# Performance work log

Measured on AMD Instinct MI355X. Metric: run time of the kernel, lower is better.

The kernel has to match this reference:

```python
import jax, jax.numpy as jnp
import numpy as np

EMBED_DIM = 1024
ZDIM = 128
STD = 0.02


def setup_inputs() -> dict:
    key = jax.random.key(0)
    ks = jax.random.split(key, 12)
    T, S, B, E, Z = 2048, 2048, 4, EMBED_DIM, ZDIM
    return {
        "query": jax.random.normal(ks[0], (T, B, E), jnp.float32),
        "key": jax.random.normal(ks[1], (S, B, E), jnp.float32),
        "Wq": jax.random.normal(ks[2], (2 * E + Z, E), jnp.float32) * STD,
        "bq": jnp.zeros((2 * E + Z,), jnp.float32),
        "Wk": jax.random.normal(ks[3], (Z, E), jnp.float32) * STD,
        "bk": jnp.zeros((Z,), jnp.float32),
        "Wv": jax.random.normal(ks[4], (E, E), jnp.float32) * STD,
        "bv": jnp.zeros((E,), jnp.float32),
        "Wh": jax.random.normal(ks[5], (E, E), jnp.float32) * STD,
        "bh": jnp.zeros((E,), jnp.float32),
        "gamma": jax.random.normal(ks[6], (2, Z), jnp.float32) * STD,
        "beta": jnp.zeros((2, Z), jnp.float32),
    }


def reference(query, key, Wq, bq, Wk, bk, Wv, bv, Wh, bh, gamma, beta):
    E, Z = EMBED_DIM, ZDIM
    scaling = Z ** (-0.5)
    # base: [T, B, 2E+Z]
    base = jnp.einsum('tbe,fe->tbf', query, Wq) + bq
    u = jax.nn.sigmoid(base[..., :E])                      # [T,B,E] output gate
    rq = jax.nn.silu(base[..., E:])                        # [T,B,E+Z]
    r = rq[..., :E]                                        # [T,B,E]
    q = rq[..., E:] * gamma[0] + beta[0]                   # [T,B,Z]
    k = jax.nn.silu(jnp.einsum('sbe,ze->sbz', key, Wk) + bk) * gamma[1] + beta[1]  # [S,B,Z]
    v = jax.nn.silu(jnp.einsum('sbe,fe->sbf', key, Wv) + bv)                       # [S,B,E]
    # softmax attention over context dim
    qk = jnp.einsum('tbz,sbz->bts', q * scaling, k)        # [B,T,S]
    attn = jax.nn.softmax(qk, axis=-1)
    h = jnp.einsum('bts,sbf->tbf', attn, v)                # [T,B,E]
    h = jnp.tanh(jnp.einsum('tbe,fe->tbf', h * r, Wh) + bh)
    out = query + u * (h - query)                          # addcmul
    return out
```

## Files before the change

kernel.cpp:

```cpp
#include <hip/hip_runtime.h>
#include <cstdint>
#include <cstddef>

using short8  = __attribute__((ext_vector_type(8))) short;
using floatx4 = __attribute__((ext_vector_type(4))) float;

#define DEV __device__ __forceinline__

DEV float u2f(unsigned short u){
  union { unsigned int i; float f; } c; c.i = ((unsigned int)u) << 16; return c.f;
}
DEV unsigned short f2u(float f){
  union { float f; unsigned int i; } c; c.f = f;
  unsigned int i = c.i;
  i += 0x7fffu + ((i >> 16) & 1u);
  return (unsigned short)(i >> 16);
}
DEV float sigmoidf_(float x){ return 1.0f / (1.0f + __expf(-x)); }
DEV float siluf_(float x){ return x / (1.0f + __expf(-x)); }

#define ASYNC_LD16(g, l) __builtin_amdgcn_global_load_lds( \
    (const __attribute__((address_space(1))) unsigned int*)(g), \
    (__attribute__((address_space(3))) unsigned int*)(l), 16, 0, 0)

constexpr float SCALING = 0.088388347648318447f;

__global__ __launch_bounds__(256) void cast_f32_bf16(
    const float* __restrict__ in, unsigned short* __restrict__ out, int n)
{
  const int i = (blockIdx.x * 256 + threadIdx.x) * 4;
  if (i >= n) return;
  const float4 v = *(const float4*)(in + i);
  ushort4 o;
  o.x = f2u(v.x); o.y = f2u(v.y); o.z = f2u(v.z); o.w = f2u(v.w);
  *(ushort4*)(out + i) = o;
}

__global__ __launch_bounds__(256) void softmax_rows(float* __restrict__ logits)
{
  const long long rb = blockIdx.x;
  float* row = logits + rb * 2048;
  unsigned short* prow = (unsigned short*)logits + rb * 4096;
  const int tid = threadIdx.x;
  const int lane = tid & 63, wv = tid >> 6;

  const float4 a = *(const float4*)(row + tid * 4);
  const float4 b = *(const float4*)(row + 1024 + tid * 4);

  float mx = fmaxf(fmaxf(fmaxf(a.x,a.y),fmaxf(a.z,a.w)),
                   fmaxf(fmaxf(b.x,b.y),fmaxf(b.z,b.w)));
  #pragma unroll
  for (int m = 32; m >= 1; m >>= 1) mx = fmaxf(mx, __shfl_xor(mx, m));
  __shared__ float red[4];
  if (lane == 0) red[wv] = mx;
  __syncthreads();
  mx = fmaxf(fmaxf(red[0], red[1]), fmaxf(red[2], red[3]));

  float e[8];
  e[0]=__expf(a.x-mx); e[1]=__expf(a.y-mx); e[2]=__expf(a.z-mx); e[3]=__expf(a.w-mx);
  e[4]=__expf(b.x-mx); e[5]=__expf(b.y-mx); e[6]=__expf(b.z-mx); e[7]=__expf(b.w-mx);
  float sm = 0.f;
  #pragma unroll
  for (int i = 0; i < 8; i++) sm += e[i];
  #pragma unroll
  for (int m = 32; m >= 1; m >>= 1) sm += __shfl_xor(sm, m);
  __syncthreads();
  if (lane == 0) red[wv] = sm;
  __syncthreads();
  const float inv = 1.0f / (red[0] + red[1] + red[2] + red[3]);

  ushort4 o0, o1;
  o0.x=f2u(e[0]*inv); o0.y=f2u(e[1]*inv); o0.z=f2u(e[2]*inv); o0.w=f2u(e[3]*inv);
  o1.x=f2u(e[4]*inv); o1.y=f2u(e[5]*inv); o1.z=f2u(e[6]*inv); o1.w=f2u(e[7]*inv);
  *(ushort4*)(prow + tid * 4) = o0;
  *(ushort4*)(prow + 1024 + tid * 4) = o1;
}

template<int EPI>
__global__ __launch_bounds__(256, 2)
void gemm_bt(const unsigned short* __restrict__ A, long long bsA, int lda,
             const unsigned short* __restrict__ Bm, long long bsB, int ldb,
             int K,
             const float* __restrict__ bias,
             const float* __restrict__ gam,
             const float* __restrict__ bet,
             float* __restrict__ f0,
             unsigned short* __restrict__ b0,
             unsigned short* __restrict__ b1,
             const unsigned short* __restrict__ rmul,
             const float* __restrict__ qin,
             const float* __restrict__ uin)
{
  __shared__ __align__(16) unsigned short As[128][64];
  __shared__ __align__(16) unsigned short Bs[128][64];

  const int tid = threadIdx.x;
  const int bm = blockIdx.x, bn = blockIdx.y, bz = blockIdx.z;
  const unsigned short* Ag = A  + (long long)bz * bsA;
  const unsigned short* Bg = Bm + (long long)bz * bsB;
  const int row0 = bm * 128;
  const int col0 = bn * 128;

  const int lane = tid & 63;
  const int wv   = tid >> 6;
  const int wm   = (wv & 1) * 64;
  const int wn   = (wv >> 1) * 64;
  const int lr   = lane & 15;
  const int lq   = lane >> 4;
  const int r7   = lr & 7;

  const unsigned short* gA[4]; const unsigned short* gB[4];
  unsigned short* lA[4]; unsigned short* lB[4];
  #pragma unroll
  for (int i = 0; i < 4; i++) {
    const int c  = tid + i * 256;
    const int rr = c >> 3;
    const int gc = (c & 7) ^ (rr & 7);
    gA[i] = Ag + (long long)(row0 + rr) * lda + gc * 8;
    gB[i] = Bg + (long long)(col0 + rr) * ldb + gc * 8;
    lA[i] = &As[0][0] + c * 8;
    lB[i] = &Bs[0][0] + c * 8;
  }

  floatx4 acc[4][4];
  const floatx4 zero = {0.f, 0.f, 0.f, 0.f};
  #pragma unroll
  for (int i = 0; i < 4; i++)
    #pragma unroll
    for (int j = 0; j < 4; j++) acc[i][j] = zero;

  for (int kt = 0; kt < K; kt += 64) {
    #pragma unroll
    for (int i = 0; i < 4; i++) {
      ASYNC_LD16(gA[i] + kt, lA[i]);
      ASYNC_LD16(gB[i] + kt, lB[i]);
    }
    __syncthreads();
    #pragma unroll
    for (int ks = 0; ks < 64; ks += 32) {
      const int k8 = ks >> 3;
      short8 af[4], bfv[4];
      #pragma unroll
      for (int i = 0; i < 4; i++) {
        const int sc = (lq + k8) ^ r7;
        af[i]  = *(const short8*)(&As[wm + i*16 + lr][sc * 8]);
        bfv[i] = *(const short8*)(&Bs[wn + i*16 + lr][sc * 8]);
      }
      #pragma unroll
      for (int mi = 0; mi < 4; mi++)
        #pragma unroll
        for (int ni = 0; ni < 4; ni++)
          acc[mi][ni] = __builtin_amdgcn_mfma_f32_16x16x32_bf16(af[mi], bfv[ni], acc[mi][ni], 0, 0, 0);
    }
    __syncthreads();
  }

  #pragma unroll
  for (int mi = 0; mi < 4; mi++) {
    #pragma unroll
    for (int ni = 0; ni < 4; ni++) {
      #pragma unroll
      for (int r = 0; r < 4; r++) {
        const int gm = row0 + wm + mi * 16 + lq * 4 + r;
        const int gn = col0 + wn + ni * 16 + lr;
        float v = acc[mi][ni][r];
        if constexpr (EPI == 0) {
          v += bias[gn];
          if (gn < 1024) {
            f0[(long long)gm * 1024 + gn] = sigmoidf_(v);
          } else if (gn < 2048) {
            b0[(long long)gm * 1024 + (gn - 1024)] = f2u(siluf_(v));
          } else {
            const int z = gn - 2048;
            b1[(long long)gm * 128 + z] = f2u(siluf_(v) * gam[z] + bet[z]);
          }
        } else if constexpr (EPI == 1) {
          v += bias[gn];
          b0[(long long)gm * 128 + gn] = f2u(siluf_(v) * gam[gn] + bet[gn]);
        } else if constexpr (EPI == 2) {
          v += bias[gn];
          const int s = gm >> 2, bb = gm & 3;
          b0[((long long)bb * 1024 + gn) * 2048 + s] = f2u(siluf_(v));
        } else if constexpr (EPI == 3) {
          f0[(long long)bz * 2048 * 2048 + (long long)gm * 2048 + gn] = v * SCALING;
        } else if constexpr (EPI == 4) {
          const long long idx = ((long long)gm * 4 + bz) * 1024 + gn;
          b0[idx] = f2u(v * u2f(rmul[idx]));
        } else {
          const long long idx = (long long)gm * 1024 + gn;
          const float tv = tanhf(v + bias[gn]);
          const float qv = qin[idx];
          f0[idx] = qv + uin[idx] * (tv - qv);
        }
      }
    }
  }
}

extern "C" void kernel_launch(void* const* d_in, const int* in_sizes, int n_in,
                              void* d_out, int out_size, void* d_ws, size_t ws_size,
                              hipStream_t stream)
{
  (void)in_sizes; (void)n_in; (void)out_size; (void)ws_size;
  const float* query = (const float*)d_in[0];
  const float* key   = (const float*)d_in[1];
  const float* Wq    = (const float*)d_in[2];
  const float* bq    = (const float*)d_in[3];
  const float* Wk    = (const float*)d_in[4];
  const float* bk    = (const float*)d_in[5];
  const float* Wv    = (const float*)d_in[6];
  const float* bv    = (const float*)d_in[7];
  const float* Wh    = (const float*)d_in[8];
  const float* bh    = (const float*)d_in[9];
  const float* gamma = (const float*)d_in[10];
  const float* beta  = (const float*)d_in[11];
  float* out = (float*)d_out;

  char* p = (char*)d_ws;
  auto take = [&](size_t bytes) -> char* {
    char* r = p; p += (bytes + 255) & ~(size_t)255; return r;
  };
  unsigned short* qbf = (unsigned short*)take(8192ULL * 1024 * 2);
  unsigned short* kbf = (unsigned short*)take(8192ULL * 1024 * 2);
  unsigned short* Wqb = (unsigned short*)take(2176ULL * 1024 * 2);
  unsigned short* Wkb = (unsigned short*)take(128ULL  * 1024 * 2);
  unsigned short* Wvb = (unsigned short*)take(1024ULL * 1024 * 2);
  unsigned short* Whb = (unsigned short*)take(1024ULL * 1024 * 2);
  float*          u_  = (float*)take(8192ULL * 1024 * 4);
  unsigned short* rbf = (unsigned short*)take(8192ULL * 1024 * 2);
  unsigned short* qpj = (unsigned short*)take(8192ULL * 128 * 2);
  unsigned short* kpj = (unsigned short*)take(8192ULL * 128 * 2);
  unsigned short* vT  = (unsigned short*)take(4ULL * 1024 * 2048 * 2);
  float*          lg  = (float*)take(4ULL * 2048 * 2048 * 4);
  unsigned short* hrb = (unsigned short*)take(8192ULL * 1024 * 2);

  dim3 blk(256);
  cast_f32_bf16<<<8192, blk, 0, stream>>>(query, qbf, 8192 * 1024);
  cast_f32_bf16<<<8192, blk, 0, stream>>>(key,   kbf, 8192 * 1024);
  cast_f32_bf16<<<2176, blk, 0, stream>>>(Wq,    Wqb, 2176 * 1024);
  cast_f32_bf16<<<128,  blk, 0, stream>>>(Wk,    Wkb, 128 * 1024);
  cast_f32_bf16<<<1024, blk, 0, stream>>>(Wv,    Wvb, 1024 * 1024);
  cast_f32_bf16<<<1024, blk, 0, stream>>>(Wh,    Whb, 1024 * 1024);

  gemm_bt<0><<<dim3(64, 17, 1), blk, 0, stream>>>(qbf, 0, 1024, Wqb, 0, 1024, 1024,
      bq, gamma, beta, u_, rbf, qpj, nullptr, nullptr, nullptr);
  gemm_bt<1><<<dim3(64, 1, 1), blk, 0, stream>>>(kbf, 0, 1024, Wkb, 0, 1024, 1024,
      bk, gamma + 128, beta + 128, nullptr, kpj, nullptr, nullptr, nullptr, nullptr);
  gemm_bt<2><<<dim3(64, 8, 1), blk, 0, stream>>>(kbf, 0, 1024, Wvb, 0, 1024, 1024,
      bv, nullptr, nullptr, nullptr, vT, nullptr, nullptr, nullptr, nullptr);
  gemm_bt<3><<<dim3(16, 16, 4), blk, 0, stream>>>(qpj, 128, 512, kpj, 128, 512, 128,
      nullptr, nullptr, nullptr, lg, nullptr, nullptr, nullptr, nullptr, nullptr);
  softmax_rows<<<8192, blk, 0, stream>>>(lg);
  gemm_bt<4><<<dim3(16, 8, 4), blk, 0, stream>>>((unsigned short*)lg, 2048LL * 4096, 4096,
      vT, 1024LL * 2048, 2048, 2048,
      nullptr, nullptr, nullptr, nullptr, hrb, nullptr, rbf, nullptr, nullptr);
  gemm_bt<5><<<dim3(64, 8, 1), blk, 0, stream>>>(hrb, 0, 1024, Whb, 0, 1024, 1024,
      bh, nullptr, nullptr, out, nullptr, nullptr, nullptr, query, u_);
}
```

Measured before the change: 395.4 us.

## Fuse softmax into QK and PV GEMM epilogues with deferred normalization

Removes the separate softmax kernel. The QK GEMM epilogue now writes exp(scaled logits) directly as bf16 and accumulates row sums with atomics. The PV GEMM divides by those row sums in its epilogue. This avoids writing fp32 logits, reading them back and rewriting them. The max-subtraction step is dropped, so exp can overflow if the logits are large. Separately, the six cast launches become two, key is rearranged into batch-major layout during the cast, and the V projection is computed transposed so the vT stores run contiguously along s.

New measurement: 457.2 us. 15.6% more time.

```diff
diff --git a/kernel.cpp b/kernel.cpp
--- a/kernel.cpp
+++ b/kernel.cpp
@@ -25,55 +25,43 @@
 
 constexpr float SCALING = 0.088388347648318447f;
 
-__global__ __launch_bounds__(256) void cast_f32_bf16(
-    const float* __restrict__ in, unsigned short* __restrict__ out, int n)
-{
-  const int i = (blockIdx.x * 256 + threadIdx.x) * 4;
-  if (i >= n) return;
-  const float4 v = *(const float4*)(in + i);
-  ushort4 o;
-  o.x = f2u(v.x); o.y = f2u(v.y); o.z = f2u(v.z); o.w = f2u(v.w);
-  *(ushort4*)(out + i) = o;
-}
-
-__global__ __launch_bounds__(256) void softmax_rows(float* __restrict__ logits)
-{
-  const long long rb = blockIdx.x;
-  float* row = logits + rb * 2048;
-  unsigned short* prow = (unsigned short*)logits + rb * 4096;
-  const int tid = threadIdx.x;
-  const int lane = tid & 63, wv = tid >> 6;
-
-  const float4 a = *(const float4*)(row + tid * 4);
-  const float4 b = *(const float4*)(row + 1024 + tid * 4);
-
-  float mx = fmaxf(fmaxf(fmaxf(a.x,a.y),fmaxf(a.z,a.w)),
-                   fmaxf(fmaxf(b.x,b.y),fmaxf(b.z,b.w)));
-  #pragma unroll
-  for (int m = 32; m >= 1; m >>= 1) mx = fmaxf(mx, __shfl_xor(mx, m));
-  __shared__ float red[4];
-  if (lane == 0) red[wv] = mx;
-  __syncthreads();
-  mx = fmaxf(fmaxf(red[0], red[1]), fmaxf(red[2], red[3]));
-
-  float e[8];
-  e[0]=__expf(a.x-mx); e[1]=__expf(a.y-mx); e[2]=__expf(a.z-mx); e[3]=__expf(a.w-mx);
-  e[4]=__expf(b.x-mx); e[5]=__expf(b.y-mx); e[6]=__expf(b.z-mx); e[7]=__expf(b.w-mx);
-  float sm = 0.f;
-  #pragma unroll
-  for (int i = 0; i < 8; i++) sm += e[i];
-  #pragma unroll
-  for (int m = 32; m >= 1; m >>= 1) sm += __shfl_xor(sm, m);
-  __syncthreads();
-  if (lane == 0) red[wv] = sm;
-  __syncthreads();
-  const float inv = 1.0f / (red[0] + red[1] + red[2] + red[3]);
-
-  ushort4 o0, o1;
-  o0.x=f2u(e[0]*inv); o0.y=f2u(e[1]*inv); o0.z=f2u(e[2]*inv); o0.w=f2u(e[3]*inv);
-  o1.x=f2u(e[4]*inv); o1.y=f2u(e[5]*inv); o1.z=f2u(e[6]*inv); o1.w=f2u(e[7]*inv);
-  *(ushort4*)(prow + tid * 4) = o0;
-  *(ushort4*)(prow + 1024 + tid * 4) = o1;
+__global__ __launch_bounds__(256) void cast_act(
+    const float* __restrict__ q, const float* __restrict__ k,
+    unsigned short* __restrict__ qo, unsigned short* __restrict__ ko)
+{
+  const int bid = blockIdx.x;
+  const int e = threadIdx.x * 4;
+  const float* src; unsigned short* dst;
+  if (bid < 8192) {
+    src = q + (long long)bid * 1024;
+    dst = qo + (long long)bid * 1024;
+  } else {
+    const int m = bid - 8192;
+    const int s = m >> 2, b = m & 3;
+    src = k + (long long)m * 1024;
+    dst = ko + ((long long)b * 2048 + s) * 1024;
+  }
+  const float4 v = *(const float4*)(src + e);
+  ushort4 o; o.x=f2u(v.x); o.y=f2u(v.y); o.z=f2u(v.z); o.w=f2u(v.w);
+  *(ushort4*)(dst + e) = o;
+}
+
+__global__ __launch_bounds__(256) void cast_w(
+    const float* __restrict__ Wq, const float* __restrict__ Wk,
+    const float* __restrict__ Wv, const float* __restrict__ Wh,
+    unsigned short* __restrict__ oq, unsigned short* __restrict__ ok,
+    unsigned short* __restrict__ ov, unsigned short* __restrict__ oh)
+{
+  const int bid = blockIdx.x;
+  const int e = threadIdx.x * 4;
+  const float* src; unsigned short* dst;
+  if (bid < 2176)      { src = Wq + (long long)bid * 1024;        dst = oq + (long long)bid * 1024; }
+  else if (bid < 2304) { src = Wk + (long long)(bid-2176) * 1024; dst = ok + (long long)(bid-2176) * 1024; }
+  else if (bid < 3328) { src = Wv + (long long)(bid-2304) * 1024; dst = ov + (long long)(bid-2304) * 1024; }
+  else                 { src = Wh + (long long)(bid-3328) * 1024; dst = oh + (long long)(bid-3328) * 1024; }
+  const float4 v = *(const float4*)(src + e);
+  ushort4 o; o.x=f2u(v.x); o.y=f2u(v.y); o.z=f2u(v.z); o.w=f2u(v.w);
+  *(ushort4*)(dst + e) = o;
 }
 
 template<int EPI>
@@ -158,39 +146,56 @@
   #pragma unroll
   for (int mi = 0; mi < 4; mi++) {
     #pragma unroll
-    for (int ni = 0; ni < 4; ni++) {
-      #pragma unroll
-      for (int r = 0; r < 4; r++) {
-        const int gm = row0 + wm + mi * 16 + lq * 4 + r;
-        const int gn = col0 + wn + ni * 16 + lr;
-        float v = acc[mi][ni][r];
-        if constexpr (EPI == 0) {
-          v += bias[gn];
-          if (gn < 1024) {
-            f0[(long long)gm * 1024 + gn] = sigmoidf_(v);
-          } else if (gn < 2048) {
-            b0[(long long)gm * 1024 + (gn - 1024)] = f2u(siluf_(v));
+    for (int r = 0; r < 4; r++) {
+      const int gm = row0 + wm + mi * 16 + lq * 4 + r;
+      if constexpr (EPI == 3) {
+        float s4 = 0.f;
+        #pragma unroll
+        for (int ni = 0; ni < 4; ni++) {
+          const int gn = col0 + wn + ni * 16 + lr;
+          const float e = __expf(acc[mi][ni][r] * SCALING);
+          b0[(long long)bz * 2048 * 2048 + (long long)gm * 2048 + gn] = f2u(e);
+          s4 += e;
+        }
+        #pragma unroll
+        for (int m2 = 8; m2 >= 1; m2 >>= 1) s4 += __shfl_xor(s4, m2);
+        if (lr == 0) atomicAdd(f0 + (long long)bz * 2048 + gm, s4);
+      } else if constexpr (EPI == 4) {
+        const float inv = 1.0f / f0[(long long)bz * 2048 + gm];
+        #pragma unroll
+        for (int ni = 0; ni < 4; ni++) {
+          const int gn = col0 + wn + ni * 16 + lr;
+          const long long idx = ((long long)gm * 4 + bz) * 1024 + gn;
+          b0[idx] = f2u(acc[mi][ni][r] * inv * u2f(rmul[idx]));
+        }
+      } else {
+        #pragma unroll
+        for (int ni = 0; ni < 4; ni++) {
+          const int gn = col0 + wn + ni * 16 + lr;
+          float v = acc[mi][ni][r];
+          if constexpr (EPI == 0) {
+            v += bias[gn];
+            if (gn < 1024) {
+              f0[(long long)gm * 1024 + gn] = sigmoidf_(v);
+            } else if (gn < 2048) {
+              b0[(long long)gm * 1024 + (gn - 1024)] = f2u(siluf_(v));
+            } else {
+              const int z = gn - 2048;
+              b1[(long long)gm * 128 + z] = f2u(siluf_(v) * gam[z] + bet[z]);
+            }
+          } else if constexpr (EPI == 1) {
+            v += bias[gn];
+            b0[(long long)gm * 128 + gn] = f2u(siluf_(v) * gam[gn] + bet[gn]);
+          } else if constexpr (EPI == 2) {
+            v += bias[gm];
+            const int b = gn >> 11, s = gn & 2047;
+            b0[((long long)b * 1024 + gm) * 2048 + s] = f2u(siluf_(v));
           } else {
-            const int z = gn - 2048;
-            b1[(long long)gm * 128 + z] = f2u(siluf_(v) * gam[z] + bet[z]);
+            const long long idx = (long long)gm * 1024 + gn;
+            const float tv = tanhf(v + bias[gn]);
+            const float qv = qin[idx];
+            f0[idx] = qv + uin[idx] * (tv - qv);
           }
-        } else if constexpr (EPI == 1) {
-          v += bias[gn];
-          b0[(long long)gm * 128 + gn] = f2u(siluf_(v) * gam[gn] + bet[gn]);
-        } else if constexpr (EPI == 2) {
-          v += bias[gn];
-          const int s = gm >> 2, bb = gm & 3;
-          b0[((long long)bb * 1024 + gn) * 2048 + s] = f2u(siluf_(v));
-        } else if constexpr (EPI == 3) {
-          f0[(long long)bz * 2048 * 2048 + (long long)gm * 2048 + gn] = v * SCALING;
-        } else if constexpr (EPI == 4) {
-          const long long idx = ((long long)gm * 4 + bz) * 1024 + gn;
-          b0[idx] = f2u(v * u2f(rmul[idx]));
-        } else {
-          const long long idx = (long long)gm * 1024 + gn;
-          const float tv = tanhf(v + bias[gn]);
-          const float qv = qin[idx];
-          f0[idx] = qv + uin[idx] * (tv - qv);
         }
       }
     }
@@ -221,7 +226,7 @@
     char* r = p; p += (bytes + 255) & ~(size_t)255; return r;
   };
   unsigned short* qbf = (unsigned short*)take(8192ULL * 1024 * 2);
-  unsigned short* kbf = (unsigned short*)take(8192ULL * 1024 * 2);
+  unsigned short* kbr = (unsigned short*)take(8192ULL * 1024 * 2);
   unsigned short* Wqb = (unsigned short*)take(2176ULL * 1024 * 2);
   unsigned short* Wkb = (unsigned short*)take(128ULL  * 1024 * 2);
   unsigned short* Wvb = (unsigned short*)take(1024ULL * 1024 * 2);
@@ -231,29 +236,26 @@
   unsigned short* qpj = (unsigned short*)take(8192ULL * 128 * 2);
   unsigned short* kpj = (unsigned short*)take(8192ULL * 128 * 2);
   unsigned short* vT  = (unsigned short*)take(4ULL * 1024 * 2048 * 2);
-  float*          lg  = (float*)take(4ULL * 2048 * 2048 * 4);
+  unsigned short* Pb  = (unsigned short*)take(4ULL * 2048 * 2048 * 2);
   unsigned short* hrb = (unsigned short*)take(8192ULL * 1024 * 2);
+  float*          rs  = (float*)take(4ULL * 2048 * 4);
 
   dim3 blk(256);
-  cast_f32_bf16<<<8192, blk, 0, stream>>>(query, qbf, 8192 * 1024);
-  cast_f32_bf16<<<8192, blk, 0, stream>>>(key,   kbf, 8192 * 1024);
-  cast_f32_bf16<<<2176, blk, 0, stream>>>(Wq,    Wqb, 2176 * 1024);
-  cast_f32_bf16<<<128,  blk, 0, stream>>>(Wk,    Wkb, 128 * 1024);
-  cast_f32_bf16<<<1024, blk, 0, stream>>>(Wv,    Wvb, 1024 * 1024);
-  cast_f32_bf16<<<1024, blk, 0, stream>>>(Wh,    Whb, 1024 * 1024);
+  cast_act<<<16384, blk, 0, stream>>>(query, key, qbf, kbr);
+  cast_w<<<4352, blk, 0, stream>>>(Wq, Wk, Wv, Wh, Wqb, Wkb, Wvb, Whb);
+  hipMemsetAsync(rs, 0, 4ULL * 2048 * 4, stream);
 
   gemm_bt<0><<<dim3(64, 17, 1), blk, 0, stream>>>(qbf, 0, 1024, Wqb, 0, 1024, 1024,
       bq, gamma, beta, u_, rbf, qpj, nullptr, nullptr, nullptr);
-  gemm_bt<1><<<dim3(64, 1, 1), blk, 0, stream>>>(kbf, 0, 1024, Wkb, 0, 1024, 1024,
+  gemm_bt<1><<<dim3(64, 1, 1), blk, 0, stream>>>(kbr, 0, 1024, Wkb, 0, 1024, 1024,
       bk, gamma + 128, beta + 128, nullptr, kpj, nullptr, nullptr, nullptr, nullptr);
-  gemm_bt<2><<<dim3(64, 8, 1), blk, 0, stream>>>(kbf, 0, 1024, Wvb, 0, 1024, 1024,
+  gemm_bt<2><<<dim3(8, 64, 1), blk, 0, stream>>>(Wvb, 0, 1024, kbr, 0, 1024, 1024,
       bv, nullptr, nullptr, nullptr, vT, nullptr, nullptr, nullptr, nullptr);
-  gemm_bt<3><<<dim3(16, 16, 4), blk, 0, stream>>>(qpj, 128, 512, kpj, 128, 512, 128,
-      nullptr, nullptr, nullptr, lg, nullptr, nullptr, nullptr, nullptr, nullptr);
-  softmax_rows<<<8192, blk, 0, stream>>>(lg);
-  gemm_bt<4><<<dim3(16, 8, 4), blk, 0, stream>>>((unsigned short*)lg, 2048LL * 4096, 4096,
+  gemm_bt<3><<<dim3(16, 16, 4), blk, 0, stream>>>(qpj, 128, 512, kpj, 2048LL * 128, 128, 128,
+      nullptr, nullptr, nullptr, rs, Pb, nullptr, nullptr, nullptr, nullptr);
+  gemm_bt<4><<<dim3(16, 8, 4), blk, 0, stream>>>(Pb, 2048LL * 2048, 2048,
       vT, 1024LL * 2048, 2048, 2048,
-      nullptr, nullptr, nullptr, nullptr, hrb, nullptr, rbf, nullptr, nullptr);
+      nullptr, nullptr, nullptr, rs, hrb, nullptr, rbf, nullptr, nullptr);
   gemm_bt<5><<<dim3(64, 8, 1), blk, 0, stream>>>(hrb, 0, 1024, Whb, 0, 1024, 1024,
       bh, nullptr, nullptr, out, nullptr, nullptr, nullptr, query, u_);
 }
```
